# Performance work log

Hardware: AMD Instinct MI355X
Metric: run time of the kernel (lower is better)

Reference implementation:

```python
import jax, jax.numpy as jnp
import numpy as np

B, S, E, G = 64, 24, 128, 256
Km, Kch, Ko, Kp, Kc = 100, 200, 50, 50, 30
Vm, Vch, Vo, Vp, Vl, Vc = 1000, 3000, 500, 1500, 700, 2000
Veth, Vgen, Vage, Vins = 10, 2, 100, 5
TOTK = Km + Kch + Ko + Kp + 1 + Kc + 4  # 435 concat width


def setup_inputs() -> dict:
    key = jax.random.key(0)
    ks = jax.random.split(key, 24)
    ri = lambda k, shape, hi: jax.random.randint(k, shape, 0, hi)
    rn = lambda k, shape: (jax.random.normal(k, shape, dtype=jnp.float32) * 0.02)
    return {
        'meds': ri(ks[0], (B, S, Km), Vm),
        'chart': ri(ks[1], (B, S, Kch), Vch),
        'out': ri(ks[2], (B, S, Ko), Vo),
        'proc': ri(ks[3], (B, S, Kp), Vp),
        'lab': ri(ks[4], (B, S), Vl),
        'conds': ri(ks[5], (B, Kc), Vc),
        'demo': ri(ks[6], (B, 4), 2),
        'med_E': rn(ks[7], (Vm, E)), 'chart_E': rn(ks[8], (Vch, E)),
        'out_E': rn(ks[9], (Vo, E)), 'proc_E': rn(ks[10], (Vp, E)),
        'lab_E': rn(ks[11], (Vl, E)), 'cond_E': rn(ks[12], (Vc, E)),
        'gender_E': rn(ks[13], (Vgen, E)), 'eth_E': rn(ks[14], (Veth, E)),
        'ins_E': rn(ks[15], (Vins, E)), 'age_E': rn(ks[16], (Vage, E)),
        'proj_W': rn(ks[17], (TOTK, E)), 'proj_b': jnp.zeros((E,), jnp.float32),
        'W1': rn(ks[18], (E, G)), 'b1': jnp.zeros((G,), jnp.float32),
        'W2': rn(ks[19], (G, G)), 'b2': jnp.zeros((G,), jnp.float32),
        'fc1_W': rn(ks[20], (G, G // 2)), 'fc1_b': jnp.zeros((G // 2,), jnp.float32),
        'fc2_W': rn(ks[21], (G // 2, 1)), 'fc2_b': jnp.zeros((1,), jnp.float32),
    }


def _forward(meds, chart, out, proc, lab, conds, demo,
             med_E, chart_E, out_E, proc_E, lab_E, cond_E,
             gender_E, eth_E, ins_E, age_E,
             proj_W, proj_b, W1, b1, W2, b2, fc1_W, fc1_b, fc2_W, fc2_b):
    clamp = lambda i, V: jnp.clip(i, 0, V - 1)
    med_e = med_E[clamp(meds, Vm)]        # [B,S,Km,E]
    chart_e = chart_E[clamp(chart, Vch)]  # [B,S,Kch,E]
    out_e = out_E[clamp(out, Vo)]         # [B,S,Ko,E]
    proc_e = proc_E[clamp(proc, Vp)]      # [B,S,Kp,E]
    lab_e = lab_E[clamp(lab, Vl)]         # [B,S,E]
    cond_e = cond_E[clamp(conds, Vc)]     # [B,Kc,E]
    gen_e = gender_E[demo[:, 0]]          # [B,E]
    eth_e = eth_E[demo[:, 1]]
    ins_e = ins_E[demo[:, 2]]
    age_e = age_E[demo[:, 3]]
    demo_cols = [jnp.broadcast_to(d[:, None, :, None], (B, S, E, 1))
                 for d in (gen_e, eth_e, ins_e, age_e)]
    x = jnp.concatenate([
        med_e.transpose(0, 1, 3, 2),    # [B,S,E,Km]
        chart_e.transpose(0, 1, 3, 2),
        out_e.transpose(0, 1, 3, 2),
        proc_e.transpose(0, 1, 3, 2),
        lab_e[..., None],               # [B,S,E,1]
        jnp.broadcast_to(cond_e[:, None], (B, S, Kc, E)).transpose(0, 1, 3, 2),
    ] + demo_cols, axis=-1)             # [B,S,E,TOTK]
    x = x.mean(axis=-2)                 # mean over embed dim -> [B,S,TOTK]
    N = B * S
    x = x.reshape(N, TOTK) @ proj_W + proj_b   # [N,E]
    # GCNConv over complete graph + self loops: normalized adjacency is 1/N
    # everywhere, so aggregation == node-mean of (x @ W).
    h = jnp.broadcast_to(jnp.mean(x @ W1, axis=0, keepdims=True) + b1, (N, G))
    h = jax.nn.relu(h)
    # entropy attention
    w = jnp.exp(-jnp.sum(h * jnp.log(h + 1e-9), axis=1))
    h = h * (w / jnp.sum(w))[:, None]
    h = jnp.broadcast_to(jnp.mean(h @ W2, axis=0, keepdims=True) + b2, (N, G))
    x_pooled = h.reshape(B, S, G).mean(axis=1)          # [B,G]
    f = jax.nn.relu(x_pooled @ fc1_W + fc1_b)           # [B,G/2]
    o = f @ fc2_W + fc2_b                               # [B,1]
    return jax.nn.sigmoid(o), o


def reference(meds, chart, out, proc, lab, conds, demo,
              med_E, chart_E, out_E, proc_E, lab_E, cond_E,
              gender_E, eth_E, ins_E, age_E,
              proj_W, proj_b, W1, b1, W2, b2, fc1_W, fc1_b, fc2_W, fc2_b):
    return _forward(meds, chart, out, proc, lab, conds, demo,
                    med_E, chart_E, out_E, proc_E, lab_E, cond_E,
                    gender_E, eth_E, ins_E, age_E,
                    proj_W, proj_b, W1, b1, W2, b2, fc1_W, fc1_b, fc2_W, fc2_b)
```

## Files before the change

kernel.cpp:

```cpp
#include <hip/hip_runtime.h>
#include <math.h>

#define B_ 64
#define S_ 24
#define E_ 128
#define G_ 256
#define N_ (B_ * S_)
#define Km_ 100
#define Kch_ 200
#define Ko_ 50
#define Kp_ 50
#define Kc_ 30
#define TOTK_ 435

#define Vm_ 1000
#define Vch_ 3000
#define Vo_ 500
#define Vp_ 1500
#define Vl_ 700
#define Vc_ 2000
#define TOTROWS_ 8817

#define OFF_MED 0
#define OFF_CHART 1000
#define OFF_OUT 4000
#define OFF_PROC 4500
#define OFF_LAB 6000
#define OFF_COND 6700
#define OFF_GEN 8700
#define OFF_ETH 8702
#define OFF_INS 8712
#define OFF_AGE 8717
#define OFF_PART 8832

#define NCHUNK_ 32
#define CHUNK_N_ 48
#define NBLK_B_ 129
#define NTHR_ 512

__device__ __forceinline__ int clampi(int v, int hi) {
    return v < 0 ? 0 : (v > hi ? hi : v);
}

__global__ __launch_bounds__(NTHR_) void rowmeans_kernel(
    const float* __restrict__ medE, const float* __restrict__ chartE,
    const float* __restrict__ outE, const float* __restrict__ procE,
    const float* __restrict__ labE, const float* __restrict__ condE,
    const float* __restrict__ genE, const float* __restrict__ ethE,
    const float* __restrict__ insE, const float* __restrict__ ageE,
    float* __restrict__ rm)
{
    int row = blockIdx.x * (NTHR_ / 64) + (threadIdx.x >> 6);
    int lane = threadIdx.x & 63;
    if (row >= TOTROWS_) return;

    const float* src;
    int r = row;
    if (r < Vm_)                  { src = medE; }
    else if ((r -= Vm_)  < Vch_)  { src = chartE; }
    else if ((r -= Vch_) < Vo_)   { src = outE; }
    else if ((r -= Vo_)  < Vp_)   { src = procE; }
    else if ((r -= Vp_)  < Vl_)   { src = labE; }
    else if ((r -= Vl_)  < Vc_)   { src = condE; }
    else if ((r -= Vc_)  < 2)     { src = genE; }
    else if ((r -= 2)    < 10)    { src = ethE; }
    else if ((r -= 10)   < 5)     { src = insE; }
    else                          { r -= 5; src = ageE; }

    float2 v = *reinterpret_cast<const float2*>(src + (size_t)r * E_ + lane * 2);
    float s = v.x + v.y;
    #pragma unroll
    for (int off = 32; off > 0; off >>= 1) s += __shfl_down(s, off, 64);
    if (lane == 0) rm[row] = s * (1.0f / E_);
}

template<int K, int RPI, int CBASE, int RMBASE, int VMAX>
__device__ __forceinline__ void table_chunk(
    const int* __restrict__ idx, const float* __restrict__ rm,
    float* __restrict__ part, int p, int t, float* __restrict__ lds)
{
    constexpr int ACT = K * RPI;
    float acc = 0.0f;
    if (t < ACT) {
        const int kk = t % K;
        const int nr = t / K;
        const int n0 = p * CHUNK_N_;
        #pragma unroll
        for (int i = 0; i < (CHUNK_N_ + RPI - 1) / RPI; ++i) {
            int n = n0 + nr + i * RPI;
            if (nr + i * RPI < CHUNK_N_) {
                int ix = clampi(idx[n * K + kk], VMAX);
                acc += rm[RMBASE + ix];
            }
        }
    }
    lds[t] = acc;
    __syncthreads();
    if (t < K) {
        float s = lds[t];
        #pragma unroll
        for (int r = 1; r < RPI; ++r) s += lds[r * K + t];
        part[(CBASE + t) * NCHUNK_ + p] = s;
    }
}

__global__ __launch_bounds__(NTHR_) void colsum_kernel(
    const int* __restrict__ meds, const int* __restrict__ chart,
    const int* __restrict__ outv, const int* __restrict__ proc,
    const int* __restrict__ lab,  const int* __restrict__ conds,
    const int* __restrict__ demo,
    const float* __restrict__ rm, float* __restrict__ part)
{
    __shared__ float lds_red[NTHR_];
    const int t = threadIdx.x;
    const int bid = blockIdx.x;

    if (bid < 128) {
        const int table = bid >> 5;
        const int p = bid & 31;
        if (table == 0)      table_chunk<Km_, 5, 0,   OFF_MED,  Vm_ -1>(meds,  rm, part, p, t, lds_red);
        else if (table == 1) table_chunk<Kch_,2, 100, OFF_CHART,Vch_-1>(chart, rm, part, p, t, lds_red);
        else if (table == 2) table_chunk<Ko_, 10,300, OFF_OUT,  Vo_ -1>(outv,  rm, part, p, t, lds_red);
        else                 table_chunk<Kp_, 10,350, OFF_PROC, Vp_ -1>(proc,  rm, part, p, t, lds_red);
    } else {
        const int lane = t & 63;
        const int w = t >> 6;
        for (int j = w; j < 35; j += 8) {
            float s = 0.0f;
            if (j == 0) {
                #pragma unroll
                for (int i = 0; i < 24; ++i)
                    s += rm[OFF_LAB + clampi(lab[lane + 64 * i], Vl_ - 1)];
            } else if (j < 31) {
                int kk = j - 1;
                s = rm[OFF_COND + clampi(conds[lane * Kc_ + kk], Vc_ - 1)];
            } else {
                int jj = j - 31;
                int base = (jj == 0) ? OFF_GEN : (jj == 1) ? OFF_ETH :
                           (jj == 2) ? OFF_INS : OFF_AGE;
                s = rm[base + demo[lane * 4 + jj]];
            }
            #pragma unroll
            for (int off = 32; off > 0; off >>= 1) s += __shfl_down(s, off, 64);
            if (lane == 0) part[(400 + j) * NCHUNK_] = s;
        }
    }
}

__global__ __launch_bounds__(NTHR_) void head_kernel(
    const float* __restrict__ part,
    const float* __restrict__ projW, const float* __restrict__ projb,
    const float* __restrict__ W1, const float* __restrict__ b1,
    const float* __restrict__ W2, const float* __restrict__ b2,
    const float* __restrict__ fc1W, const float* __restrict__ fc1b,
    const float* __restrict__ fc2W, const float* __restrict__ fc2b,
    float* __restrict__ outp)
{
    __shared__ float sm[TOTK_];
    __shared__ float xbar[E_];
    __shared__ float h1s[G_];
    __shared__ float h2s[G_];
    __shared__ float fsh[G_ / 2];
    __shared__ float4 red4[16][32];
    __shared__ float4 part4[8][64];
    __shared__ float hred[8];
    __shared__ float oval;

    const int t = threadIdx.x;
    const int lane = t & 63;
    const int oc = t >> 6;

    const float4* W1p = (const float4*)W1;
    float4 w1r[16];
    {
        const int k0 = oc * 16;
        #pragma unroll
        for (int i = 0; i < 16; ++i)
            w1r[i] = W1p[(k0 + i) * 64 + lane];
    }

    if (t < TOTK_) {
        const float4* pp = (const float4*)(part + t * NCHUNK_);
        float s;
        if (t < 400) {
            s = 0.f;
            #pragma unroll
            for (int j = 0; j < NCHUNK_ / 4; ++j) {
                float4 v = pp[j];
                s += (v.x + v.y) + (v.z + v.w);
            }
            s *= (1.0f / N_);
        } else if (t == 400) {
            s = part[t * NCHUNK_] * (1.0f / N_);
        } else {
            s = part[t * NCHUNK_] * (1.0f / B_);
        }
        sm[t] = s;
    }
    __syncthreads();

    {
        const float4* Wp = (const float4*)projW;
        const int c4 = t & 31;
        const int kg = t >> 5;
        const int k0 = kg * 28;
        float4 acc = {0.f, 0.f, 0.f, 0.f};
        #pragma unroll
        for (int i = 0; i < 28; ++i) {
            int k = k0 + i;
            if (k < TOTK_) {
                float s = sm[k];
                float4 w = Wp[k * 32 + c4];
                acc.x += s * w.x; acc.y += s * w.y; acc.z += s * w.z; acc.w += s * w.w;
            }
        }
        red4[kg][c4] = acc;
        __syncthreads();
        if (t < 32) {
            float4 a = red4[0][t];
            #pragma unroll
            for (int j = 1; j < 16; ++j) {
                float4 p = red4[j][t];
                a.x += p.x; a.y += p.y; a.z += p.z; a.w += p.w;
            }
            float4 bb = ((const float4*)projb)[t];
            xbar[4 * t]     = a.x + bb.x;
            xbar[4 * t + 1] = a.y + bb.y;
            xbar[4 * t + 2] = a.z + bb.z;
            xbar[4 * t + 3] = a.w + bb.w;
        }
        __syncthreads();
    }

    {
        const int k0 = oc * 16;
        float4 acc = {0.f, 0.f, 0.f, 0.f};
        #pragma unroll
        for (int i = 0; i < 16; ++i) {
            float s = xbar[k0 + i];
            float4 w = w1r[i];
            acc.x += s * w.x; acc.y += s * w.y; acc.z += s * w.z; acc.w += s * w.w;
        }
        part4[oc][lane] = acc;
        __syncthreads();
        if (t < 64) {
            float4 a = part4[0][t];
            #pragma unroll
            for (int j = 1; j < 8; ++j) {
                float4 p = part4[j][t];
                a.x += p.x; a.y += p.y; a.z += p.z; a.w += p.w;
            }
            float4 bb = ((const float4*)b1)[t];
            h1s[4 * t]     = fmaxf(a.x + bb.x, 0.f) * (1.0f / N_);
            h1s[4 * t + 1] = fmaxf(a.y + bb.y, 0.f) * (1.0f / N_);
            h1s[4 * t + 2] = fmaxf(a.z + bb.z, 0.f) * (1.0f / N_);
            h1s[4 * t + 3] = fmaxf(a.w + bb.w, 0.f) * (1.0f / N_);
        }
        __syncthreads();
    }

    {
        const float4* Wp = (const float4*)W2;
        const int k0 = oc * 32, k1 = k0 + 32;
        float4 acc = {0.f, 0.f, 0.f, 0.f};
        #pragma unroll 8
        for (int k = k0; k < k1; ++k) {
            float s = h1s[k];
            float4 w = Wp[k * 64 + lane];
            acc.x += s * w.x; acc.y += s * w.y; acc.z += s * w.z; acc.w += s * w.w;
        }
        part4[oc][lane] = acc;
        __syncthreads();
        if (t < 64) {
            float4 a = part4[0][t];
            #pragma unroll
            for (int j = 1; j < 8; ++j) {
                float4 p = part4[j][t];
                a.x += p.x; a.y += p.y; a.z += p.z; a.w += p.w;
            }
            float4 bb = ((const float4*)b2)[t];
            h2s[4 * t]     = a.x + bb.x;
            h2s[4 * t + 1] = a.y + bb.y;
            h2s[4 * t + 2] = a.z + bb.z;
            h2s[4 * t + 3] = a.w + bb.w;
        }
        __syncthreads();
    }

    {
        const float4* Wp = (const float4*)fc1W;
        const int c4 = t & 31;
        const int kg = t >> 5;
        const int k0 = kg * 16;
        float4 acc = {0.f, 0.f, 0.f, 0.f};
        #pragma unroll 8
        for (int i = 0; i < 16; ++i) {
            int k = k0 + i;
            float s = h2s[k];
            float4 w = Wp[k * 32 + c4];
            acc.x += s * w.x; acc.y += s * w.y; acc.z += s * w.z; acc.w += s * w.w;
        }
        red4[kg][c4] = acc;
        __syncthreads();
        if (t < 32) {
            float4 a = red4[0][t];
            #pragma unroll
            for (int j = 1; j < 16; ++j) {
                float4 p = red4[j][t];
                a.x += p.x; a.y += p.y; a.z += p.z; a.w += p.w;
            }
            float4 bb = ((const float4*)fc1b)[t];
            fsh[4 * t]     = fmaxf(a.x + bb.x, 0.f);
            fsh[4 * t + 1] = fmaxf(a.y + bb.y, 0.f);
            fsh[4 * t + 2] = fmaxf(a.z + bb.z, 0.f);
            fsh[4 * t + 3] = fmaxf(a.w + bb.w, 0.f);
        }
        __syncthreads();
    }

    {
        float p = (t < G_ / 2) ? fsh[t] * fc2W[t] : 0.f;
        #pragma unroll
        for (int off = 32; off > 0; off >>= 1) p += __shfl_down(p, off, 64);
        if (lane == 0) hred[oc] = p;
        __syncthreads();
        if (t == 0) {
            float o = fc2b[0];
            #pragma unroll
            for (int j = 0; j < 8; ++j) o += hred[j];
            oval = o;
        }
        __syncthreads();
        const float o = oval;
        const float sig = 1.0f / (1.0f + expf(-o));
        if (t < B_)            outp[t] = sig;
        else if (t < 2 * B_)   outp[t] = o;
    }
}

extern "C" void kernel_launch(void* const* d_in, const int* in_sizes, int n_in,
                              void* d_out, int out_size, void* d_ws, size_t ws_size,
                              hipStream_t stream) {
    const int* meds  = (const int*)d_in[0];
    const int* chart = (const int*)d_in[1];
    const int* outv  = (const int*)d_in[2];
    const int* proc  = (const int*)d_in[3];
    const int* lab   = (const int*)d_in[4];
    const int* conds = (const int*)d_in[5];
    const int* demo  = (const int*)d_in[6];
    const float* medE   = (const float*)d_in[7];
    const float* chartE = (const float*)d_in[8];
    const float* outE   = (const float*)d_in[9];
    const float* procE  = (const float*)d_in[10];
    const float* labE   = (const float*)d_in[11];
    const float* condE  = (const float*)d_in[12];
    const float* genE   = (const float*)d_in[13];
    const float* ethE   = (const float*)d_in[14];
    const float* insE   = (const float*)d_in[15];
    const float* ageE   = (const float*)d_in[16];
    const float* projW  = (const float*)d_in[17];
    const float* projb  = (const float*)d_in[18];
    const float* W1     = (const float*)d_in[19];
    const float* b1     = (const float*)d_in[20];
    const float* W2     = (const float*)d_in[21];
    const float* b2     = (const float*)d_in[22];
    const float* fc1W   = (const float*)d_in[23];
    const float* fc1b   = (const float*)d_in[24];
    const float* fc2W   = (const float*)d_in[25];
    const float* fc2b   = (const float*)d_in[26];

    float* rm   = (float*)d_ws;
    float* part = (float*)d_ws + OFF_PART;
    float* outp = (float*)d_out;

    int blocksA = (TOTROWS_ + (NTHR_ / 64) - 1) / (NTHR_ / 64);
    rowmeans_kernel<<<blocksA, NTHR_, 0, stream>>>(
        medE, chartE, outE, procE, labE, condE, genE, ethE, insE, ageE, rm);

    colsum_kernel<<<NBLK_B_, NTHR_, 0, stream>>>(
        meds, chart, outv, proc, lab, conds, demo, rm, part);

    head_kernel<<<1, NTHR_, 0, stream>>>(
        part, projW, projb, W1, b1, W2, b2, fc1W, fc1b, fc2W, fc2b, outp);
}
```

Before: 25.25 us.

## Convert head weights to bf16 in first kernel to halve single-block head loads

Extra blocks added to the row-means kernel convert projW, W1, W2 and fc1W from fp32 to bf16 in workspace, running in parallel with the existing row work. The single-block head kernel then reads the bf16 copies and widens them to fp32 before the matvecs. This halves the bytes the latency-bound one-block head kernel must fetch. In exchange every call pays for an extra conversion pass over about 186K weights, and the bf16 rounding reduces precision.

```diff
diff --git a/kernel.cpp b/kernel.cpp
--- a/kernel.cpp
+++ b/kernel.cpp
@@ -32,14 +32,65 @@
 #define OFF_INS 8712
 #define OFF_AGE 8717
 #define OFF_PART 8832
+#define OFF_WB   22752
+
+#define WB_PROJ 0
+#define WB_W1   55680
+#define WB_W2   88448
+#define WB_FC1  153984
+#define WB_TOT  186752
 
 #define NCHUNK_ 32
 #define CHUNK_N_ 48
 #define NBLK_B_ 129
 #define NTHR_ 512
 
+#define NBLKA_ROWS_ ((TOTROWS_ + 7) / 8)
+#define NBLKA_CVT_ 24
+
 __device__ __forceinline__ int clampi(int v, int hi) {
     return v < 0 ? 0 : (v > hi ? hi : v);
+}
+
+__device__ __forceinline__ unsigned short f2bf(float f) {
+    union { float f; unsigned int u; } v; v.f = f;
+    unsigned int u = v.u;
+    u += 0x7fffu + ((u >> 16) & 1u);
+    return (unsigned short)(u >> 16);
+}
+__device__ __forceinline__ float bf2f(unsigned short u) {
+    union { unsigned int i; float f; } v; v.i = ((unsigned int)u) << 16; return v.f;
+}
+__device__ __forceinline__ float4 bf2f4(ushort4 w) {
+    float4 r;
+    r.x = bf2f(w.x); r.y = bf2f(w.y); r.z = bf2f(w.z); r.w = bf2f(w.w);
+    return r;
+}
+
+__device__ void convert_body(
+    int cb, int t,
+    const float* __restrict__ projW, const float* __restrict__ W1,
+    const float* __restrict__ W2,   const float* __restrict__ fc1W,
+    unsigned short* __restrict__ wb)
+{
+    const float* srcs[4] = {projW, W1, W2, fc1W};
+    const int n4s[4]  = {55680 / 4, 32768 / 4, 65536 / 4, 32768 / 4};
+    const int dsts[4] = {WB_PROJ, WB_W1, WB_W2, WB_FC1};
+    #pragma unroll
+    for (int a = 0; a < 4; ++a) {
+        const float4* s = (const float4*)srcs[a];
+        unsigned short* d = wb + dsts[a];
+        const int n4 = n4s[a];
+        const int chunk = (n4 + NBLKA_CVT_ - 1) / NBLKA_CVT_;
+        const int i0 = cb * chunk;
+        const int i1 = (i0 + chunk < n4) ? i0 + chunk : n4;
+        for (int i = i0 + t; i < i1; i += NTHR_) {
+            float4 v = s[i];
+            ushort4 o;
+            o.x = f2bf(v.x); o.y = f2bf(v.y); o.z = f2bf(v.z); o.w = f2bf(v.w);
+            *reinterpret_cast<ushort4*>(d + i * 4) = o;
+        }
+    }
 }
 
 __global__ __launch_bounds__(NTHR_) void rowmeans_kernel(
@@ -48,8 +99,15 @@
     const float* __restrict__ labE, const float* __restrict__ condE,
     const float* __restrict__ genE, const float* __restrict__ ethE,
     const float* __restrict__ insE, const float* __restrict__ ageE,
-    float* __restrict__ rm)
+    const float* __restrict__ projW, const float* __restrict__ W1,
+    const float* __restrict__ W2,   const float* __restrict__ fc1W,
+    float* __restrict__ rm, unsigned short* __restrict__ wb)
 {
+    if (blockIdx.x >= NBLKA_ROWS_) {
+        convert_body(blockIdx.x - NBLKA_ROWS_, threadIdx.x, projW, W1, W2, fc1W, wb);
+        return;
+    }
+
     int row = blockIdx.x * (NTHR_ / 64) + (threadIdx.x >> 6);
     int lane = threadIdx.x & 63;
     if (row >= TOTROWS_) return;
@@ -149,11 +207,10 @@
 
 __global__ __launch_bounds__(NTHR_) void head_kernel(
     const float* __restrict__ part,
-    const float* __restrict__ projW, const float* __restrict__ projb,
-    const float* __restrict__ W1, const float* __restrict__ b1,
-    const float* __restrict__ W2, const float* __restrict__ b2,
-    const float* __restrict__ fc1W, const float* __restrict__ fc1b,
-    const float* __restrict__ fc2W, const float* __restrict__ fc2b,
+    const unsigned short* __restrict__ wb,
+    const float* __restrict__ projb, const float* __restrict__ b1,
+    const float* __restrict__ b2,    const float* __restrict__ fc1b,
+    const float* __restrict__ fc2W,  const float* __restrict__ fc2b,
     float* __restrict__ outp)
 {
     __shared__ float sm[TOTK_];
@@ -170,13 +227,17 @@
     const int lane = t & 63;
     const int oc = t >> 6;
 
-    const float4* W1p = (const float4*)W1;
+    const ushort4* projWp = (const ushort4*)(wb + WB_PROJ);
+    const ushort4* W1p    = (const ushort4*)(wb + WB_W1);
+    const ushort4* W2p    = (const ushort4*)(wb + WB_W2);
+    const ushort4* fc1Wp  = (const ushort4*)(wb + WB_FC1);
+
     float4 w1r[16];
     {
         const int k0 = oc * 16;
         #pragma unroll
         for (int i = 0; i < 16; ++i)
-            w1r[i] = W1p[(k0 + i) * 64 + lane];
+            w1r[i] = bf2f4(W1p[(k0 + i) * 64 + lane]);
     }
 
     if (t < TOTK_) {
@@ -200,7 +261,6 @@
     __syncthreads();
 
     {
-        const float4* Wp = (const float4*)projW;
         const int c4 = t & 31;
         const int kg = t >> 5;
         const int k0 = kg * 28;
@@ -210,7 +270,7 @@
             int k = k0 + i;
             if (k < TOTK_) {
                 float s = sm[k];
-                float4 w = Wp[k * 32 + c4];
+                float4 w = bf2f4(projWp[k * 32 + c4]);
                 acc.x += s * w.x; acc.y += s * w.y; acc.z += s * w.z; acc.w += s * w.w;
             }
         }
@@ -260,13 +320,12 @@
     }
 
     {
-        const float4* Wp = (const float4*)W2;
         const int k0 = oc * 32, k1 = k0 + 32;
         float4 acc = {0.f, 0.f, 0.f, 0.f};
         #pragma unroll 8
         for (int k = k0; k < k1; ++k) {
             float s = h1s[k];
-            float4 w = Wp[k * 64 + lane];
+            float4 w = bf2f4(W2p[k * 64 + lane]);
             acc.x += s * w.x; acc.y += s * w.y; acc.z += s * w.z; acc.w += s * w.w;
         }
         part4[oc][lane] = acc;
@@ -288,7 +347,6 @@
     }
 
     {
-        const float4* Wp = (const float4*)fc1W;
         const int c4 = t & 31;
         const int kg = t >> 5;
         const int k0 = kg * 16;
@@ -297,7 +355,7 @@
         for (int i = 0; i < 16; ++i) {
             int k = k0 + i;
             float s = h2s[k];
-            float4 w = Wp[k * 32 + c4];
+            float4 w = bf2f4(fc1Wp[k * 32 + c4]);
             acc.x += s * w.x; acc.y += s * w.y; acc.z += s * w.z; acc.w += s * w.w;
         }
         red4[kg][c4] = acc;
@@ -371,15 +429,16 @@
 
     float* rm   = (float*)d_ws;
     float* part = (float*)d_ws + OFF_PART;
+    unsigned short* wb = (unsigned short*)((float*)d_ws + OFF_WB);
     float* outp = (float*)d_out;
 
-    int blocksA = (TOTROWS_ + (NTHR_ / 64) - 1) / (NTHR_ / 64);
-    rowmeans_kernel<<<blocksA, NTHR_, 0, stream>>>(
-        medE, chartE, outE, procE, labE, condE, genE, ethE, insE, ageE, rm);
+    rowmeans_kernel<<<NBLKA_ROWS_ + NBLKA_CVT_, NTHR_, 0, stream>>>(
+        medE, chartE, outE, procE, labE, condE, genE, ethE, insE, ageE,
+        projW, W1, W2, fc1W, rm, wb);
 
     colsum_kernel<<<NBLK_B_, NTHR_, 0, stream>>>(
         meds, chart, outv, proc, lab, conds, demo, rm, part);
 
     head_kernel<<<1, NTHR_, 0, stream>>>(
-        part, projW, projb, W1, b1, W2, b2, fc1W, fc1b, fc2W, fc2b, outp);
-}
+        part, wb, projb, b1, b2, fc1b, fc2W, fc2b, outp);
+}
```

After: 32.68 us. +29.4%, slower.
